# Optimization experiments

Measured on AMD Instinct MI355X. Metric: run time of the kernel, lower is better.

The kernel has to match this reference:

```python
import jax, jax.numpy as jnp
import numpy as np
from jax import lax

PERCENT_T = 0.1
BN_EPS = 1e-5


def setup_inputs() -> dict:
    key = jax.random.key(0)
    ks = jax.random.split(key, 4)
    B, C, H, W = 32, 512, 56, 56
    R = C // 16
    x = jax.random.normal(ks[0], (B, C, H, W), dtype=jnp.float32)
    w1 = jax.random.normal(ks[1], (R, C), dtype=jnp.float32) * (1.0 / np.sqrt(C))
    b1 = jnp.zeros((R,), dtype=jnp.float32)
    w2 = jax.random.normal(ks[2], (C, R), dtype=jnp.float32) * (1.0 / np.sqrt(R))
    b2 = jnp.zeros((C,), dtype=jnp.float32)
    conv_w = jax.random.normal(ks[3], (1, 2, 7, 7), dtype=jnp.float32) * 0.1
    bn_gamma = jnp.ones((1,), dtype=jnp.float32)
    bn_beta = jnp.zeros((1,), dtype=jnp.float32)
    bn_mean = jnp.zeros((1,), dtype=jnp.float32)
    bn_var = jnp.ones((1,), dtype=jnp.float32)
    return {"x": x, "w1": w1, "b1": b1, "w2": w2, "b2": b2,
            "conv_w": conv_w, "bn_gamma": bn_gamma, "bn_beta": bn_beta,
            "bn_mean": bn_mean, "bn_var": bn_var}


def reference(x, w1, b1, w2, b2, conv_w, bn_gamma, bn_beta, bn_mean, bn_var):
    b, c, h, w = x.shape
    hw = h * w
    top_t = int(round(hw * PERCENT_T))  # static at trace time

    # --- TopTPercentChannelGate ---
    x_flat = x.reshape(b, c, hw)
    sel, _ = lax.top_k(x_flat, top_t)            # [b, c, top_t]
    pool_avg = sel.mean(axis=2)                  # [b, c]
    pool_max = sel.max(axis=2)                   # [b, c]

    def mlp(p):  # p: [b, c]
        h1 = jax.nn.relu(p @ w1.T + b1)
        return h1 @ w2.T + b2

    att = mlp(pool_avg) + mlp(pool_max)          # [b, c]
    x_out = x * jax.nn.sigmoid(att)[:, :, None, None]

    # --- SpatialGate ---
    cp = jnp.stack([x_out.max(axis=1), x_out.mean(axis=1)], axis=1)  # [b, 2, h, w]
    conv = lax.conv_general_dilated(
        cp, conv_w, window_strides=(1, 1), padding=[(3, 3), (3, 3)],
        dimension_numbers=("NCHW", "OIHW", "NCHW"))                   # [b, 1, h, w]
    bn = ((conv - bn_mean[None, :, None, None])
          * lax.rsqrt(bn_var[None, :, None, None] + BN_EPS)
          * bn_gamma[None, :, None, None] + bn_beta[None, :, None, None])
    return x_out * jax.nn.sigmoid(bn)
```

## Files before the change

kernel.cpp:

```cpp
#include <hip/hip_runtime.h>
#include <math.h>

#define NB 32
#define NC 512
#define NH 56
#define NW 56
#define NHW 3136
#define TOPT 314
#define NR 32
#define RBUCK 2048

typedef float f32x4 __attribute__((ext_vector_type(4)));

__device__ __forceinline__ unsigned int f2s(float f) {
    unsigned int b = __float_as_uint(f);
    return (b & 0x80000000u) ? ~b : (b | 0x80000000u);
}
__device__ __forceinline__ float s2f(unsigned int u) {
    unsigned int b = (u & 0x80000000u) ? (u ^ 0x80000000u) : ~u;
    return __uint_as_float(b);
}

__global__ __launch_bounds__(256) void topk_pool_kernel(
        const float* __restrict__ x,
        float* __restrict__ pool_avg, float* __restrict__ pool_max) {
    __shared__ unsigned int hist[2][RBUCK];
    __shared__ unsigned int wtot[4];
    __shared__ unsigned int sh_pref[2], sh_k[2];
    __shared__ float redsA[4], redsB[4];
    __shared__ unsigned int redmA[4], redmB[4];

    const int rowA = blockIdx.x * 2;
    const int tid = threadIdx.x;
    const int wid = tid >> 6;
    const int lane = tid & 63;
    const float* xa = x + (size_t)rowA * NHW;
    const float* xb = xa + NHW;
    const float4* xa4 = (const float4*)xa;
    const float4* xb4 = (const float4*)xb;

    float4 a0 = xa4[tid], a1 = xa4[256 + tid], a2 = xa4[512 + tid];
    float4 b0 = xb4[tid], b1 = xb4[256 + tid], b2 = xb4[512 + tid];
    const bool has13 = (tid < 64);
    float exA = has13 ? xa[3072 + tid] : 0.f;
    float exB = has13 ? xb[3072 + tid] : 0.f;

    unsigned int u[13], w[13];
    u[0] = f2s(a0.x); u[1] = f2s(a0.y); u[2]  = f2s(a0.z); u[3]  = f2s(a0.w);
    u[4] = f2s(a1.x); u[5] = f2s(a1.y); u[6]  = f2s(a1.z); u[7]  = f2s(a1.w);
    u[8] = f2s(a2.x); u[9] = f2s(a2.y); u[10] = f2s(a2.z); u[11] = f2s(a2.w);
    u[12] = f2s(exA);
    w[0] = f2s(b0.x); w[1] = f2s(b0.y); w[2]  = f2s(b0.z); w[3]  = f2s(b0.w);
    w[4] = f2s(b1.x); w[5] = f2s(b1.y); w[6]  = f2s(b1.z); w[7]  = f2s(b1.w);
    w[8] = f2s(b2.x); w[9] = f2s(b2.y); w[10] = f2s(b2.z); w[11] = f2s(b2.w);
    w[12] = f2s(exB);

    unsigned int prefA = 0u, prefB = 0u, mask = 0u;
    unsigned int kA = TOPT, kB = TOPT;
    const int shifts[3] = {21, 10, 0};
    #pragma unroll
    for (int r = 0; r < 3; ++r) {
        const int shift = shifts[r];
        {
            uint4 z = make_uint4(0u, 0u, 0u, 0u);
            uint4* h0 = (uint4*)hist[0];
            h0[tid] = z; h0[256 + tid] = z;
            if (r == 0) {
                uint4* h1 = (uint4*)hist[1];
                h1[tid] = z; h1[256 + tid] = z;
            }
        }
        __syncthreads();
        unsigned int* h = (r == 0) ? hist[wid >> 1] : hist[0];
        #pragma unroll
        for (int j = 0; j < 13; ++j) {
            const bool live = (j < 12) || has13;
            if (live && ((u[j] & mask) == prefA))
                atomicAdd(&h[(u[j] >> shift) & (RBUCK - 1u)], 1u);
            if (live && ((w[j] & mask) == prefB))
                atomicAdd(&h[(w[j] >> shift) & (RBUCK - 1u)], 65536u);
        }
        __syncthreads();

        unsigned int vv[8];
        unsigned int g = 0u;
        if (r == 0) {
            #pragma unroll
            for (int bb = 0; bb < 8; ++bb) {
                vv[bb] = hist[0][8 * tid + bb] + hist[1][8 * tid + bb];
                g += vv[bb];
            }
        } else {
            #pragma unroll
            for (int bb = 0; bb < 8; ++bb) { vv[bb] = hist[0][8 * tid + bb]; g += vv[bb]; }
        }
        unsigned int S = g;
        #pragma unroll
        for (int off = 1; off < 64; off <<= 1) {
            unsigned int t2 = __shfl_down(S, off);
            if (lane + off < 64) S += t2;
        }
        if (lane == 0) wtot[wid] = S;
        __syncthreads();
        unsigned int hi = 0u;
        if (wid < 3) hi += wtot[wid + 1];
        if (wid < 2) hi += wtot[wid + 2];
        if (wid < 1) hi += wtot[wid + 3];
        S += hi;
        const unsigned int SloT = S & 0xFFFFu, ShiT = S >> 16;
        const unsigned int gLo = g & 0xFFFFu,  gHi = g >> 16;
        const unsigned int aboveLo = SloT - gLo, aboveHi = ShiT - gHi;
        if (SloT >= kA && aboveLo < kA) {
            unsigned int cum = aboveLo;
            #pragma unroll
            for (int bb = 7; bb >= 0; --bb) {
                const unsigned int hh = vv[bb] & 0xFFFFu;
                if (cum + hh >= kA) {
                    sh_pref[0] = prefA | ((unsigned int)(8 * tid + bb) << shift);
                    sh_k[0] = kA - cum;
                    break;
                }
                cum += hh;
            }
        }
        if (ShiT >= kB && aboveHi < kB) {
            unsigned int cum = aboveHi;
            #pragma unroll
            for (int bb = 7; bb >= 0; --bb) {
                const unsigned int hh = vv[bb] >> 16;
                if (cum + hh >= kB) {
                    sh_pref[1] = prefB | ((unsigned int)(8 * tid + bb) << shift);
                    sh_k[1] = kB - cum;
                    break;
                }
                cum += hh;
            }
        }
        __syncthreads();
        prefA = sh_pref[0]; kA = sh_k[0];
        prefB = sh_pref[1]; kB = sh_k[1];
        mask = 0xFFFFFFFFu << shift;
    }

    const unsigned int tA = prefA, tB = prefB;
    float sumA = 0.f, sumB = 0.f;
    unsigned int mA = 0u, mB = 0u;
    #pragma unroll
    for (int j = 0; j < 13; ++j) {
        const bool live = (j < 12) || has13;
        if (live) {
            mA = max(mA, u[j]);
            if (u[j] > tA) sumA += s2f(u[j]);
            mB = max(mB, w[j]);
            if (w[j] > tB) sumB += s2f(w[j]);
        }
    }
    #pragma unroll
    for (int off = 32; off > 0; off >>= 1) {
        sumA += __shfl_down(sumA, off);
        sumB += __shfl_down(sumB, off);
        mA = max(mA, __shfl_down(mA, off));
        mB = max(mB, __shfl_down(mB, off));
    }
    if (lane == 0) { redsA[wid] = sumA; redsB[wid] = sumB;
                     redmA[wid] = mA;   redmB[wid] = mB; }
    __syncthreads();
    if (tid == 0) {
        float totA = redsA[0] + redsA[1] + redsA[2] + redsA[3] + (float)kA * s2f(tA);
        float totB = redsB[0] + redsB[1] + redsB[2] + redsB[3] + (float)kB * s2f(tB);
        pool_avg[rowA]     = totA * (1.0f / (float)TOPT);
        pool_avg[rowA + 1] = totB * (1.0f / (float)TOPT);
        pool_max[rowA]     = s2f(max(max(redmA[0], redmA[1]), max(redmA[2], redmA[3])));
        pool_max[rowA + 1] = s2f(max(max(redmB[0], redmB[1]), max(redmB[2], redmB[3])));
    }
}

__global__ __launch_bounds__(256) void mlp_kernel(
        const float* __restrict__ pool_avg, const float* __restrict__ pool_max,
        const float* __restrict__ w1, const float* __restrict__ b1,
        const float* __restrict__ w2, const float* __restrict__ b2,
        float* __restrict__ s_out) {
    __shared__ float pa[NC], pm[NC], h1a[NR], h1m[NR];
    const int b = blockIdx.x, tid = threadIdx.x;
    for (int c = tid; c < NC; c += 256) {
        pa[c] = pool_avg[b * NC + c];
        pm[c] = pool_max[b * NC + c];
    }
    __syncthreads();
    if (tid < 64) {
        const int r = tid & 31;
        const float* wrow = w1 + r * NC;
        const float* p = (tid < 32) ? pa : pm;
        float acc = b1[r];
        for (int c = 0; c < NC; ++c) acc += p[c] * wrow[c];
        float h = fmaxf(acc, 0.f);
        if (tid < 32) h1a[r] = h; else h1m[r] = h;
    }
    __syncthreads();
    for (int c = tid; c < NC; c += 256) {
        float acc = 2.f * b2[c];
        const float* wrow = w2 + c * NR;
        for (int r = 0; r < NR; ++r) acc += (h1a[r] + h1m[r]) * wrow[r];
        s_out[b * NC + c] = 1.f / (1.f + expf(-acc));
    }
}

__global__ __launch_bounds__(256) void spatial_pool_kernel(
        const float* __restrict__ x, const float* __restrict__ s,
        float* __restrict__ cp_max, float* __restrict__ cp_avg) {
    __shared__ float sc[NC];
    __shared__ float4 pmx[7][32];
    __shared__ float4 psm[7][32];
    const int b = blockIdx.y, tid = threadIdx.x;
    const int qo = tid & 31;
    const int cg = tid >> 5;
    const int q = blockIdx.x * 32 + qo;
    for (int c = tid; c < NC; c += 256) sc[c] = s[b * NC + c];
    __syncthreads();
    const float4* xb4 = (const float4*)(x + (size_t)b * NC * NHW);
    float4 mx = make_float4(-INFINITY, -INFINITY, -INFINITY, -INFINITY);
    float4 sm = make_float4(0.f, 0.f, 0.f, 0.f);
    const bool valid = (q < NHW / 4);
    if (valid) {
        #pragma unroll 2
        for (int c = cg * 64; c < cg * 64 + 64; ++c) {
            float4 v = xb4[(size_t)c * (NHW / 4) + q];
            const float scv = sc[c];
            v.x *= scv; v.y *= scv; v.z *= scv; v.w *= scv;
            mx.x = fmaxf(mx.x, v.x); mx.y = fmaxf(mx.y, v.y);
            mx.z = fmaxf(mx.z, v.z); mx.w = fmaxf(mx.w, v.w);
            sm.x += v.x; sm.y += v.y; sm.z += v.z; sm.w += v.w;
        }
    }
    if (cg > 0 && valid) { pmx[cg - 1][qo] = mx; psm[cg - 1][qo] = sm; }
    __syncthreads();
    if (cg == 0 && valid) {
        #pragma unroll
        for (int i = 0; i < 7; ++i) {
            const float4 m2 = pmx[i][qo];
            const float4 s2 = psm[i][qo];
            mx.x = fmaxf(mx.x, m2.x); mx.y = fmaxf(mx.y, m2.y);
            mx.z = fmaxf(mx.z, m2.z); mx.w = fmaxf(mx.w, m2.w);
            sm.x += s2.x; sm.y += s2.y; sm.z += s2.z; sm.w += s2.w;
        }
        const float inv = 1.0f / (float)NC;
        sm.x *= inv; sm.y *= inv; sm.z *= inv; sm.w *= inv;
        ((float4*)(cp_max + b * NHW))[q] = mx;
        ((float4*)(cp_avg + b * NHW))[q] = sm;
    }
}

__global__ __launch_bounds__(256) void conv_gate_kernel(
        const float* __restrict__ cp_max, const float* __restrict__ cp_avg,
        const float* __restrict__ conv_w,
        const float* __restrict__ gamma, const float* __restrict__ beta,
        const float* __restrict__ mean, const float* __restrict__ var,
        float* __restrict__ g) {
    __shared__ float wgt[98];
    const int b = blockIdx.y, tid = threadIdx.x;
    const int p = blockIdx.x * 256 + tid;
    if (tid < 98) wgt[tid] = conv_w[tid];
    __syncthreads();
    if (p >= NHW) return;
    const int h = p / NW, w = p - h * NW;
    const float* cm = cp_max + b * NHW;
    const float* ca = cp_avg + b * NHW;
    float acc = 0.f;
    for (int i = 0; i < 7; ++i) {
        const int hh = h - 3 + i;
        if (hh < 0 || hh >= NH) continue;
        for (int j = 0; j < 7; ++j) {
            const int ww = w - 3 + j;
            if (ww < 0 || ww >= NW) continue;
            const int q = hh * NW + ww;
            acc += cm[q] * wgt[i * 7 + j] + ca[q] * wgt[49 + i * 7 + j];
        }
    }
    const float bnv = (acc - mean[0]) * rsqrtf(var[0] + 1e-5f) * gamma[0] + beta[0];
    g[b * NHW + p] = 1.f / (1.f + expf(-bnv));
}

__global__ __launch_bounds__(256) void scale_out_kernel(
        const float* __restrict__ x, const float* __restrict__ s,
        const float* __restrict__ g, float* __restrict__ out) {
    const int bc = blockIdx.x;
    const int b = bc >> 9;
    const int tid = threadIdx.x;
    const float sv = s[bc];
    const f32x4* xr = (const f32x4*)(x + (size_t)bc * NHW);
    const f32x4* gr = (const f32x4*)(g + (size_t)b * NHW);
    f32x4* orow = (f32x4*)(out + (size_t)bc * NHW);
    #pragma unroll
    for (int i = 0; i < 3; ++i) {
        const int q = tid + 256 * i;
        f32x4 xv = xr[q];
        f32x4 gv = gr[q];
        f32x4 ov = xv * sv * gv;
        __builtin_nontemporal_store(ov, &orow[q]);
    }
    if (tid < 16) {
        const int q = 768 + tid;
        f32x4 xv = xr[q];
        f32x4 gv = gr[q];
        f32x4 ov = xv * sv * gv;
        __builtin_nontemporal_store(ov, &orow[q]);
    }
}

extern "C" void kernel_launch(void* const* d_in, const int* in_sizes, int n_in,
                              void* d_out, int out_size, void* d_ws, size_t ws_size,
                              hipStream_t stream) {
    const float* x      = (const float*)d_in[0];
    const float* w1     = (const float*)d_in[1];
    const float* b1     = (const float*)d_in[2];
    const float* w2     = (const float*)d_in[3];
    const float* b2     = (const float*)d_in[4];
    const float* conv_w = (const float*)d_in[5];
    const float* gamma  = (const float*)d_in[6];
    const float* beta   = (const float*)d_in[7];
    const float* mean   = (const float*)d_in[8];
    const float* var    = (const float*)d_in[9];
    float* out = (float*)d_out;

    float* ws = (float*)d_ws;
    float* pool_avg = ws;
    float* pool_max = ws + 16384;
    float* s        = ws + 32768;
    float* cp_max   = ws + 49152;
    float* cp_avg   = ws + 149504;
    float* g        = ws + 249856;

    topk_pool_kernel<<<NB * NC / 2, 256, 0, stream>>>(x, pool_avg, pool_max);
    mlp_kernel<<<NB, 256, 0, stream>>>(pool_avg, pool_max, w1, b1, w2, b2, s);
    dim3 grid3((NHW / 4 + 31) / 32, NB);
    spatial_pool_kernel<<<grid3, 256, 0, stream>>>(x, s, cp_max, cp_avg);
    dim3 grid4((NHW + 255) / 256, NB);
    conv_gate_kernel<<<grid4, 256, 0, stream>>>(cp_max, cp_avg, conv_w,
                                                gamma, beta, mean, var, g);
    scale_out_kernel<<<NB * NC, 256, 0, stream>>>(x, s, g, out);
}
```

Before: 176.8 us.

## Prefilter top-k radix histogram with mean+sigma threshold and permute histogram layout

```diff
diff --git a/kernel.cpp b/kernel.cpp
--- a/kernel.cpp
+++ b/kernel.cpp
@@ -9,6 +9,8 @@
 #define TOPT 314
 #define NR 32
 #define RBUCK 2048
+#define HWORDS 2112
+#define HPERM(b) (((b) >> 3) + 264u * ((b) & 7u))
 
 typedef float f32x4 __attribute__((ext_vector_type(4)));
 
@@ -24,9 +26,11 @@
 __global__ __launch_bounds__(256) void topk_pool_kernel(
         const float* __restrict__ x,
         float* __restrict__ pool_avg, float* __restrict__ pool_max) {
-    __shared__ unsigned int hist[2][RBUCK];
+    __shared__ unsigned int hist[2][HWORDS];
     __shared__ unsigned int wtot[4];
     __shared__ unsigned int sh_pref[2], sh_k[2];
+    __shared__ float shst[4][4];
+    __shared__ unsigned int shc[4];
     __shared__ float redsA[4], redsB[4];
     __shared__ unsigned int redmA[4], redmB[4];
 
@@ -44,6 +48,18 @@
     const bool has13 = (tid < 64);
     float exA = has13 ? xa[3072 + tid] : 0.f;
     float exB = has13 ? xb[3072 + tid] : 0.f;
+
+    float sA = 0.f, qA = 0.f, sB = 0.f, qB = 0.f;
+#define ACCA(v) { sA += (v); qA = fmaf((v), (v), qA); }
+#define ACCB(v) { sB += (v); qB = fmaf((v), (v), qB); }
+    ACCA(a0.x) ACCA(a0.y) ACCA(a0.z) ACCA(a0.w)
+    ACCA(a1.x) ACCA(a1.y) ACCA(a1.z) ACCA(a1.w)
+    ACCA(a2.x) ACCA(a2.y) ACCA(a2.z) ACCA(a2.w) ACCA(exA)
+    ACCB(b0.x) ACCB(b0.y) ACCB(b0.z) ACCB(b0.w)
+    ACCB(b1.x) ACCB(b1.y) ACCB(b1.z) ACCB(b1.w)
+    ACCB(b2.x) ACCB(b2.y) ACCB(b2.z) ACCB(b2.w) ACCB(exB)
+#undef ACCA
+#undef ACCB
 
     unsigned int u[13], w[13];
     u[0] = f2s(a0.x); u[1] = f2s(a0.y); u[2]  = f2s(a0.z); u[3]  = f2s(a0.w);
@@ -55,6 +71,42 @@
     w[8] = f2s(b2.x); w[9] = f2s(b2.y); w[10] = f2s(b2.z); w[11] = f2s(b2.w);
     w[12] = f2s(exB);
 
+    #pragma unroll
+    for (int off = 32; off > 0; off >>= 1) {
+        sA += __shfl_down(sA, off); qA += __shfl_down(qA, off);
+        sB += __shfl_down(sB, off); qB += __shfl_down(qB, off);
+    }
+    if (lane == 0) { shst[wid][0] = sA; shst[wid][1] = qA;
+                     shst[wid][2] = sB; shst[wid][3] = qB; }
+    __syncthreads();
+    const float inv_n = 1.0f / (float)NHW;
+    float SAt = shst[0][0] + shst[1][0] + shst[2][0] + shst[3][0];
+    float QAt = shst[0][1] + shst[1][1] + shst[2][1] + shst[3][1];
+    float SBt = shst[0][2] + shst[1][2] + shst[2][2] + shst[3][2];
+    float QBt = shst[0][3] + shst[1][3] + shst[2][3] + shst[3][3];
+    const float muA = SAt * inv_n, muB = SBt * inv_n;
+    const float sgA = sqrtf(fmaxf(QAt * inv_n - muA * muA, 0.f));
+    const float sgB = sqrtf(fmaxf(QBt * inv_n - muB * muB, 0.f));
+    unsigned int BA = f2s(fmaf(1.1f, sgA, muA)) & 0xFFE00000u;
+    unsigned int BB = f2s(fmaf(1.1f, sgB, muB)) & 0xFFE00000u;
+
+    unsigned int cnt = 0u;
+    #pragma unroll
+    for (int j = 0; j < 13; ++j) {
+        const bool live = (j < 12) || has13;
+        if (live) {
+            cnt += (u[j] >= BA) ? 1u : 0u;
+            cnt += (w[j] >= BB) ? 65536u : 0u;
+        }
+    }
+    #pragma unroll
+    for (int off = 32; off > 0; off >>= 1) cnt += __shfl_down(cnt, off);
+    if (lane == 0) shc[wid] = cnt;
+    __syncthreads();
+    const unsigned int ctot = shc[0] + shc[1] + shc[2] + shc[3];
+    if ((ctot & 0xFFFFu) < TOPT) BA = 0u;
+    if ((ctot >> 16) < TOPT) BB = 0u;
+
     unsigned int prefA = 0u, prefB = 0u, mask = 0u;
     unsigned int kA = TOPT, kB = TOPT;
     const int shifts[3] = {21, 10, 0};
@@ -66,19 +118,32 @@
             uint4* h0 = (uint4*)hist[0];
             h0[tid] = z; h0[256 + tid] = z;
             if (r == 0) {
-                uint4* h1 = (uint4*)hist[1];
-                h1[tid] = z; h1[256 + tid] = z;
+                h0[512 + tid] = z; h0[768 + tid] = z;
+                if (tid < 32) h0[1024 + tid] = z;
+            } else if (tid < 16) {
+                h0[512 + tid] = z;
             }
         }
         __syncthreads();
         unsigned int* h = (r == 0) ? hist[wid >> 1] : hist[0];
-        #pragma unroll
-        for (int j = 0; j < 13; ++j) {
-            const bool live = (j < 12) || has13;
-            if (live && ((u[j] & mask) == prefA))
-                atomicAdd(&h[(u[j] >> shift) & (RBUCK - 1u)], 1u);
-            if (live && ((w[j] & mask) == prefB))
-                atomicAdd(&h[(w[j] >> shift) & (RBUCK - 1u)], 65536u);
+        if (r == 0) {
+            #pragma unroll
+            for (int j = 0; j < 13; ++j) {
+                const bool live = (j < 12) || has13;
+                if (live && (u[j] >= BA))
+                    atomicAdd(&h[HPERM((u[j] >> 21))], 1u);
+                if (live && (w[j] >= BB))
+                    atomicAdd(&h[HPERM((w[j] >> 21))], 65536u);
+            }
+        } else {
+            #pragma unroll
+            for (int j = 0; j < 13; ++j) {
+                const bool live = (j < 12) || has13;
+                if (live && ((u[j] & mask) == prefA))
+                    atomicAdd(&h[HPERM(((u[j] >> shift) & (RBUCK - 1u)))], 1u);
+                if (live && ((w[j] & mask) == prefB))
+                    atomicAdd(&h[HPERM(((w[j] >> shift) & (RBUCK - 1u)))], 65536u);
+            }
         }
         __syncthreads();
 
@@ -87,12 +152,12 @@
         if (r == 0) {
             #pragma unroll
             for (int bb = 0; bb < 8; ++bb) {
-                vv[bb] = hist[0][8 * tid + bb] + hist[1][8 * tid + bb];
+                vv[bb] = hist[0][tid + 264 * bb] + hist[1][tid + 264 * bb];
                 g += vv[bb];
             }
         } else {
             #pragma unroll
-            for (int bb = 0; bb < 8; ++bb) { vv[bb] = hist[0][8 * tid + bb]; g += vv[bb]; }
+            for (int bb = 0; bb < 8; ++bb) { vv[bb] = hist[0][tid + 264 * bb]; g += vv[bb]; }
         }
         unsigned int S = g;
         #pragma unroll
```

Result: slower. 186.0 us (+5.2%).

## Prune negative values in first radix pass and split MLP first layer across threads

Applied to the files above, without the earlier changes.

```diff
diff --git a/kernel.cpp b/kernel.cpp
--- a/kernel.cpp
+++ b/kernel.cpp
@@ -9,6 +9,7 @@
 #define TOPT 314
 #define NR 32
 #define RBUCK 2048
+#define SENT 0xFFFFFFFFu
 
 typedef float f32x4 __attribute__((ext_vector_type(4)));
 
@@ -55,45 +56,110 @@
     w[8] = f2s(b2.x); w[9] = f2s(b2.y); w[10] = f2s(b2.z); w[11] = f2s(b2.w);
     w[12] = f2s(exB);
 
-    unsigned int prefA = 0u, prefB = 0u, mask = 0u;
-    unsigned int kA = TOPT, kB = TOPT;
-    const int shifts[3] = {21, 10, 0};
+    unsigned int prefA, prefB, kA, kB;
+
+    bool pruned = true;
+    for (;;) {
+        {
+            uint4 z = make_uint4(0u, 0u, 0u, 0u);
+            uint4* h0 = (uint4*)hist[0];
+            uint4* h1 = (uint4*)hist[1];
+            h0[tid] = z; h0[256 + tid] = z;
+            h1[tid] = z; h1[256 + tid] = z;
+        }
+        if (tid == 0) { sh_k[0] = SENT; sh_k[1] = SENT; }
+        __syncthreads();
+        unsigned int* h = hist[wid >> 1];
+        #pragma unroll
+        for (int j = 0; j < 13; ++j) {
+            const bool live = (j < 12) || has13;
+            if (live && (!pruned || (u[j] & 0x80000000u)))
+                atomicAdd(&h[u[j] >> 21], 1u);
+            if (live && (!pruned || (w[j] & 0x80000000u)))
+                atomicAdd(&h[w[j] >> 21], 65536u);
+        }
+        __syncthreads();
+        unsigned int vv[8];
+        unsigned int g = 0u;
+        #pragma unroll
+        for (int bb = 0; bb < 8; ++bb) {
+            vv[bb] = hist[0][8 * tid + bb] + hist[1][8 * tid + bb];
+            g += vv[bb];
+        }
+        unsigned int S = g;
+        #pragma unroll
+        for (int off = 1; off < 64; off <<= 1) {
+            unsigned int t2 = __shfl_down(S, off);
+            if (lane + off < 64) S += t2;
+        }
+        if (lane == 0) wtot[wid] = S;
+        __syncthreads();
+        unsigned int hi = 0u;
+        if (wid < 3) hi += wtot[wid + 1];
+        if (wid < 2) hi += wtot[wid + 2];
+        if (wid < 1) hi += wtot[wid + 3];
+        S += hi;
+        const unsigned int SloT = S & 0xFFFFu, ShiT = S >> 16;
+        const unsigned int gLo = g & 0xFFFFu,  gHi = g >> 16;
+        const unsigned int aboveLo = SloT - gLo, aboveHi = ShiT - gHi;
+        if (SloT >= TOPT && aboveLo < TOPT) {
+            unsigned int cum = aboveLo;
+            #pragma unroll
+            for (int bb = 7; bb >= 0; --bb) {
+                const unsigned int hh = vv[bb] & 0xFFFFu;
+                if (cum + hh >= TOPT) {
+                    sh_pref[0] = (unsigned int)(8 * tid + bb) << 21;
+                    sh_k[0] = TOPT - cum;
+                    break;
+                }
+                cum += hh;
+            }
+        }
+        if (ShiT >= TOPT && aboveHi < TOPT) {
+            unsigned int cum = aboveHi;
+            #pragma unroll
+            for (int bb = 7; bb >= 0; --bb) {
+                const unsigned int hh = vv[bb] >> 16;
+                if (cum + hh >= TOPT) {
+                    sh_pref[1] = (unsigned int)(8 * tid + bb) << 21;
+                    sh_k[1] = TOPT - cum;
+                    break;
+                }
+                cum += hh;
+            }
+        }
+        __syncthreads();
+        if (sh_k[0] != SENT && sh_k[1] != SENT) break;
+        pruned = false;
+    }
+    prefA = sh_pref[0]; kA = sh_k[0];
+    prefB = sh_pref[1]; kB = sh_k[1];
+
+    const int shifts2[2] = {10, 0};
+    const unsigned int masks2[2] = {0xFFE00000u, 0xFFFFFC00u};
     #pragma unroll
-    for (int r = 0; r < 3; ++r) {
-        const int shift = shifts[r];
+    for (int r = 0; r < 2; ++r) {
+        const int shift = shifts2[r];
+        const unsigned int mask = masks2[r];
         {
             uint4 z = make_uint4(0u, 0u, 0u, 0u);
             uint4* h0 = (uint4*)hist[0];
             h0[tid] = z; h0[256 + tid] = z;
-            if (r == 0) {
-                uint4* h1 = (uint4*)hist[1];
-                h1[tid] = z; h1[256 + tid] = z;
-            }
-        }
-        __syncthreads();
-        unsigned int* h = (r == 0) ? hist[wid >> 1] : hist[0];
+        }
+        __syncthreads();
         #pragma unroll
         for (int j = 0; j < 13; ++j) {
             const bool live = (j < 12) || has13;
             if (live && ((u[j] & mask) == prefA))
-                atomicAdd(&h[(u[j] >> shift) & (RBUCK - 1u)], 1u);
+                atomicAdd(&hist[0][(u[j] >> shift) & (RBUCK - 1u)], 1u);
             if (live && ((w[j] & mask) == prefB))
-                atomicAdd(&h[(w[j] >> shift) & (RBUCK - 1u)], 65536u);
-        }
-        __syncthreads();
-
+                atomicAdd(&hist[0][(w[j] >> shift) & (RBUCK - 1u)], 65536u);
+        }
+        __syncthreads();
         unsigned int vv[8];
         unsigned int g = 0u;
-        if (r == 0) {
-            #pragma unroll
-            for (int bb = 0; bb < 8; ++bb) {
-                vv[bb] = hist[0][8 * tid + bb] + hist[1][8 * tid + bb];
-                g += vv[bb];
-            }
-        } else {
-            #pragma unroll
-            for (int bb = 0; bb < 8; ++bb) { vv[bb] = hist[0][8 * tid + bb]; g += vv[bb]; }
-        }
+        #pragma unroll
+        for (int bb = 0; bb < 8; ++bb) { vv[bb] = hist[0][8 * tid + bb]; g += vv[bb]; }
         unsigned int S = g;
         #pragma unroll
         for (int off = 1; off < 64; off <<= 1) {
@@ -139,7 +205,6 @@
         __syncthreads();
         prefA = sh_pref[0]; kA = sh_k[0];
         prefB = sh_pref[1]; kB = sh_k[1];
-        mask = 0xFFFFFFFFu << shift;
     }
 
     const unsigned int tA = prefA, tB = prefB;
@@ -180,19 +245,29 @@
         const float* __restrict__ w1, const float* __restrict__ b1,
         const float* __restrict__ w2, const float* __restrict__ b2,
         float* __restrict__ s_out) {
-    __shared__ float pa[NC], pm[NC], h1a[NR], h1m[NR];
+    __shared__ float pa[NC], pm[NC], part[64][4], h1a[NR], h1m[NR];
     const int b = blockIdx.x, tid = threadIdx.x;
     for (int c = tid; c < NC; c += 256) {
         pa[c] = pool_avg[b * NC + c];
         pm[c] = pool_max[b * NC + c];
     }
     __syncthreads();
+    {
+        const int r = tid & 31;
+        const int half = (tid >> 5) & 1;
+        const int seg = tid >> 6;
+        const float* p = (half ? pm : pa) + seg * 128;
+        const float* wrow = w1 + r * NC + seg * 128;
+        float acc = 0.f;
+        #pragma unroll 4
+        for (int c = 0; c < 128; ++c) acc = fmaf(p[c], wrow[c], acc);
+        part[tid & 63][seg] = acc;
+    }
+    __syncthreads();
     if (tid < 64) {
         const int r = tid & 31;
-        const float* wrow = w1 + r * NC;
-        const float* p = (tid < 32) ? pa : pm;
-        float acc = b1[r];
-        for (int c = 0; c < NC; ++c) acc += p[c] * wrow[c];
+        float acc = b1[r] + part[tid][0] + part[tid][1]
+                  + part[tid][2] + part[tid][3];
         float h = fmaxf(acc, 0.f);
         if (tid < 32) h1a[r] = h; else h1m[r] = h;
     }
```

Measured after the change: 182.2 us. 3.0% more time.
